# Kernel optimization log

Hardware: AMD Instinct MI355X
Metric: run time of the kernel (lower is better)

## Reference

```python
import jax, jax.numpy as jnp
import numpy as np

BS, N, D = 4, 512, 128

def setup_inputs() -> dict:
    key = jax.random.key(0)
    ks = jax.random.split(key, 8)
    s = 1.0 / np.sqrt(D)
    return {
        "x":  jax.random.normal(ks[0], (BS, N, D), dtype=jnp.float32),
        "Wq": jax.random.normal(ks[1], (D, D), dtype=jnp.float32) * s,
        "bq": jax.random.normal(ks[2], (D,), dtype=jnp.float32) * s,
        "Wk": jax.random.normal(ks[3], (D, D), dtype=jnp.float32) * s,
        "bk": jax.random.normal(ks[4], (D,), dtype=jnp.float32) * s,
        "Wv": jax.random.normal(ks[5], (D, D), dtype=jnp.float32) * s,
        "bv": jax.random.normal(ks[6], (D,), dtype=jnp.float32) * s,
        "pos_bias": jax.random.normal(ks[7], (N, N), dtype=jnp.float32) * 0.1,
    }

def reference(x, Wq, bq, Wk, bk, Wv, bv, pos_bias):
    # Linear projections (torch Linear: x @ W^T + b)
    q = jax.nn.sigmoid(jnp.einsum('bnd,ed->bne', x, Wq) + bq)   # [B,N,D]
    k = jnp.einsum('bnd,ed->bne', x, Wk) + bk                   # [B,N,D]
    v = jnp.einsum('bnd,ed->bne', x, Wv) + bv                   # [B,N,D]
    # scores[b,t,j,d] = k[b,j,d] + pos_bias[t,j]  (O(n^2 d) intermediate)
    s = k[:, None, :, :] + pos_bias[None, :, :, None]           # [B,N,N,D]
    m = jnp.max(s, axis=2, keepdims=True)                       # stabilizer
    e = jnp.exp(s - m)                                          # [B,N,N,D]
    num = jnp.einsum('btjd,bjd->btd', e, v)                     # [B,N,D]
    den = jnp.sum(e, axis=2)                                    # [B,N,D]
    return q * (num / den)
```

## Files before the change

kernel.cpp:

```cpp
#include <hip/hip_runtime.h>

#define BATCH 4
#define SEQ   512
#define DIM   128

typedef _Float16 half8 __attribute__((ext_vector_type(8)));
typedef _Float16 half4 __attribute__((ext_vector_type(4)));
typedef float    f32x4 __attribute__((ext_vector_type(4)));

__device__ __forceinline__ half8 ld8h(const float* __restrict__ p) {
    const float4 a = *(const float4*)p;
    const float4 b = *(const float4*)(p + 4);
    half8 h;
    h[0] = (_Float16)a.x; h[1] = (_Float16)a.y; h[2] = (_Float16)a.z; h[3] = (_Float16)a.w;
    h[4] = (_Float16)b.x; h[5] = (_Float16)b.y; h[6] = (_Float16)b.z; h[7] = (_Float16)b.w;
    return h;
}

__global__ __launch_bounds__(256) void KA(
    const float* __restrict__ x,
    const float* __restrict__ Wq, const float* __restrict__ bq,
    const float* __restrict__ Wk, const float* __restrict__ bk,
    const float* __restrict__ Wv, const float* __restrict__ bv,
    const float* __restrict__ pos,
    float* __restrict__ qout, _Float16* __restrict__ ekk,
    _Float16* __restrict__ ep_h)
{
    const int tid = threadIdx.x;
    const int bi  = blockIdx.x;

    if (bi >= 256) {
        const int i = ((bi - 256) * 256 + tid) * 8;
        const float4 p0 = *(const float4*)(pos + i);
        const float4 p1 = *(const float4*)(pos + i + 4);
        half8 h;
        h[0] = (_Float16)__expf(p0.x); h[1] = (_Float16)__expf(p0.y);
        h[2] = (_Float16)__expf(p0.z); h[3] = (_Float16)__expf(p0.w);
        h[4] = (_Float16)__expf(p1.x); h[5] = (_Float16)__expf(p1.y);
        h[6] = (_Float16)__expf(p1.z); h[7] = (_Float16)__expf(p1.w);
        *(half8*)(ep_h + i) = h;
        return;
    }

    const int lane = tid & 63;
    const int wave = tid >> 6;
    const int l15  = lane & 15;
    const int quad = lane >> 4;

    const int n0 = (bi & 7) * 16;
    const int m0 = (bi >> 3) * 64 + wave * 16;

    const float* xa = x  + (m0 + l15) * DIM + quad * 8;
    const float* wq = Wq + (n0 + l15) * DIM + quad * 8;
    const float* wk = Wk + (n0 + l15) * DIM + quad * 8;
    const float* wv = Wv + (n0 + l15) * DIM + quad * 8;

    f32x4 aq = {0.f, 0.f, 0.f, 0.f};
    f32x4 ak = {0.f, 0.f, 0.f, 0.f};
    f32x4 av = {0.f, 0.f, 0.f, 0.f};

#pragma unroll
    for (int ks = 0; ks < 4; ++ks) {
        const half8 a  = ld8h(xa + ks * 32);
        const half8 b0 = ld8h(wq + ks * 32);
        const half8 b1 = ld8h(wk + ks * 32);
        const half8 b2 = ld8h(wv + ks * 32);
        aq = __builtin_amdgcn_mfma_f32_16x16x32_f16(a, b0, aq, 0, 0, 0);
        ak = __builtin_amdgcn_mfma_f32_16x16x32_f16(a, b1, ak, 0, 0, 0);
        av = __builtin_amdgcn_mfma_f32_16x16x32_f16(a, b2, av, 0, 0, 0);
    }

    const int c = n0 + l15;
    const float bqv = bq[c];
    const float bkv = bk[c];
    const float bvv = bv[c];

    const int mrow = m0 + quad * 4;
    const int b    = mrow >> 9;
    const int tok  = mrow & 511;

    half4 eh, evh;
#pragma unroll
    for (int r = 0; r < 4; ++r) {
        const float e  = __expf(ak[r] + bkv);
        const float vv = av[r] + bvv;
        const float qv = 1.f / (1.f + __expf(-(aq[r] + bqv)));
        eh[r]  = (_Float16)e;
        evh[r] = (_Float16)(e * vv);
        qout[(b * SEQ + tok + r) * DIM + c] = qv;
    }
    *(half4*)(ekk + ((b * 256) + 2 * c + 0) * SEQ + tok) = eh;
    *(half4*)(ekk + ((b * 256) + 2 * c + 1) * SEQ + tok) = evh;
}

__global__ __launch_bounds__(256) void KB(
    const _Float16* __restrict__ ekk,
    const _Float16* __restrict__ ep_h,
    const float* __restrict__ qout,
    float* __restrict__ out)
{
    const int tid  = threadIdx.x;
    const int lane = tid & 63;
    const int wave = tid >> 6;
    const int l15  = lane & 15;
    const int quad = lane >> 4;

    const int bi = blockIdx.x;
    const int b  = bi >> 7;
    const int mt = (bi >> 4) & 7;
    const int tt = bi & 15;

    const int m0 = mt * 32 + (wave & 1) * 16;
    const int t0 = tt * 32 + (wave >> 1) * 16;

    const _Float16* arow = ekk  + ((b * 256) + m0 + l15) * SEQ + quad * 8;
    const _Float16* brow = ep_h + (t0 + l15) * SEQ + quad * 8;

    f32x4 acc = {0.f, 0.f, 0.f, 0.f};

#pragma unroll
    for (int ks = 0; ks < 16; ++ks) {
        const half8 a  = *(const half8*)(arow + ks * 32);
        const half8 b8 = *(const half8*)(brow + ks * 32);
        acc = __builtin_amdgcn_mfma_f32_16x16x32_f16(a, b8, acc, 0, 0, 0);
    }

    const int d0 = (m0 + quad * 4) >> 1;
    const int t  = t0 + l15;
    const float2 qv = *(const float2*)(qout + ((b * SEQ) + t) * DIM + d0);
    float2 o;
    o.x = qv.x * acc[1] / acc[0];
    o.y = qv.y * acc[3] / acc[2];
    *(float2*)(out + ((b * SEQ) + t) * DIM + d0) = o;
}

extern "C" void kernel_launch(void* const* d_in, const int* in_sizes, int n_in,
                              void* d_out, int out_size, void* d_ws, size_t ws_size,
                              hipStream_t stream) {
    const float* x   = (const float*)d_in[0];
    const float* Wq  = (const float*)d_in[1];
    const float* bq  = (const float*)d_in[2];
    const float* Wk  = (const float*)d_in[3];
    const float* bk  = (const float*)d_in[4];
    const float* Wv  = (const float*)d_in[5];
    const float* bv  = (const float*)d_in[6];
    const float* pos = (const float*)d_in[7];

    float* outp = (float*)d_out;
    char*  ws   = (char*)d_ws;

    _Float16* ekk  = (_Float16*)(ws);
    _Float16* ep_h = (_Float16*)(ws + (1024 << 10));
    float*    qout = (float*)   (ws + (1536 << 10));

    KA<<<384, 256, 0, stream>>>(x, Wq, bq, Wk, bk, Wv, bv, pos, qout, ekk, ep_h);
    KB<<<512, 256, 0, stream>>>(ekk, ep_h, qout, outp);
}
```

Before: 81.16 us.

## Fuse projection, exp and attention-sum into one kernel using LDS staging

Merges the two kernels into one. Each block recomputes exp(K) and exp(K)*V for its batch and 16-dim slice over all tokens, plus exp(pos_bias) for its 32 query rows, and stages them in padded shared memory before the MFMA reduction. This removes the global workspace round trip and a second launch. The cost is redundant recomputation of the K/V projection across the 16 query tiles, heavy L2 traffic for x, and large LDS use that limits occupancy.

```diff
diff --git a/kernel.cpp b/kernel.cpp
--- a/kernel.cpp
+++ b/kernel.cpp
@@ -3,6 +3,7 @@
 #define BATCH 4
 #define SEQ   512
 #define DIM   128
+#define PADJ  516
 
 typedef _Float16 half8 __attribute__((ext_vector_type(8)));
 typedef _Float16 half4 __attribute__((ext_vector_type(4)));
@@ -17,121 +18,137 @@
     return h;
 }
 
-__global__ __launch_bounds__(256) void KA(
+__global__ __launch_bounds__(256, 2) void k_fused(
     const float* __restrict__ x,
     const float* __restrict__ Wq, const float* __restrict__ bq,
     const float* __restrict__ Wk, const float* __restrict__ bk,
     const float* __restrict__ Wv, const float* __restrict__ bv,
     const float* __restrict__ pos,
-    float* __restrict__ qout, _Float16* __restrict__ ekk,
-    _Float16* __restrict__ ep_h)
-{
-    const int tid = threadIdx.x;
-    const int bi  = blockIdx.x;
-
-    if (bi >= 256) {
-        const int i = ((bi - 256) * 256 + tid) * 8;
-        const float4 p0 = *(const float4*)(pos + i);
-        const float4 p1 = *(const float4*)(pos + i + 4);
-        half8 h;
-        h[0] = (_Float16)__expf(p0.x); h[1] = (_Float16)__expf(p0.y);
-        h[2] = (_Float16)__expf(p0.z); h[3] = (_Float16)__expf(p0.w);
-        h[4] = (_Float16)__expf(p1.x); h[5] = (_Float16)__expf(p1.y);
-        h[6] = (_Float16)__expf(p1.z); h[7] = (_Float16)__expf(p1.w);
-        *(half8*)(ep_h + i) = h;
-        return;
-    }
-
-    const int lane = tid & 63;
-    const int wave = tid >> 6;
-    const int l15  = lane & 15;
-    const int quad = lane >> 4;
-
-    const int n0 = (bi & 7) * 16;
-    const int m0 = (bi >> 3) * 64 + wave * 16;
-
-    const float* xa = x  + (m0 + l15) * DIM + quad * 8;
-    const float* wq = Wq + (n0 + l15) * DIM + quad * 8;
-    const float* wk = Wk + (n0 + l15) * DIM + quad * 8;
-    const float* wv = Wv + (n0 + l15) * DIM + quad * 8;
-
-    f32x4 aq = {0.f, 0.f, 0.f, 0.f};
-    f32x4 ak = {0.f, 0.f, 0.f, 0.f};
-    f32x4 av = {0.f, 0.f, 0.f, 0.f};
-
-#pragma unroll
-    for (int ks = 0; ks < 4; ++ks) {
-        const half8 a  = ld8h(xa + ks * 32);
-        const half8 b0 = ld8h(wq + ks * 32);
-        const half8 b1 = ld8h(wk + ks * 32);
-        const half8 b2 = ld8h(wv + ks * 32);
-        aq = __builtin_amdgcn_mfma_f32_16x16x32_f16(a, b0, aq, 0, 0, 0);
-        ak = __builtin_amdgcn_mfma_f32_16x16x32_f16(a, b1, ak, 0, 0, 0);
-        av = __builtin_amdgcn_mfma_f32_16x16x32_f16(a, b2, av, 0, 0, 0);
-    }
-
-    const int c = n0 + l15;
-    const float bqv = bq[c];
-    const float bkv = bk[c];
-    const float bvv = bv[c];
-
-    const int mrow = m0 + quad * 4;
-    const int b    = mrow >> 9;
-    const int tok  = mrow & 511;
-
-    half4 eh, evh;
-#pragma unroll
-    for (int r = 0; r < 4; ++r) {
-        const float e  = __expf(ak[r] + bkv);
-        const float vv = av[r] + bvv;
-        const float qv = 1.f / (1.f + __expf(-(aq[r] + bqv)));
-        eh[r]  = (_Float16)e;
-        evh[r] = (_Float16)(e * vv);
-        qout[(b * SEQ + tok + r) * DIM + c] = qv;
-    }
-    *(half4*)(ekk + ((b * 256) + 2 * c + 0) * SEQ + tok) = eh;
-    *(half4*)(ekk + ((b * 256) + 2 * c + 1) * SEQ + tok) = evh;
-}
-
-__global__ __launch_bounds__(256) void KB(
-    const _Float16* __restrict__ ekk,
-    const _Float16* __restrict__ ep_h,
-    const float* __restrict__ qout,
     float* __restrict__ out)
 {
+    __shared__ _Float16 ekk_s[32 * PADJ];
+    __shared__ _Float16 ep_s [32 * PADJ];
+    __shared__ float    q_s  [32 * 16];
+
     const int tid  = threadIdx.x;
     const int lane = tid & 63;
     const int wave = tid >> 6;
     const int l15  = lane & 15;
     const int quad = lane >> 4;
 
-    const int bi = blockIdx.x;
-    const int b  = bi >> 7;
-    const int mt = (bi >> 4) & 7;
-    const int tt = bi & 15;
+    const int bi  = blockIdx.x;
+    const int b   = bi >> 7;
+    const int dt  = (bi >> 4) & 7;
+    const int tt  = bi & 15;
+    const int d0g = dt * 16;
+    const int t0g = tt * 32;
 
-    const int m0 = mt * 32 + (wave & 1) * 16;
-    const int t0 = tt * 32 + (wave >> 1) * 16;
+    const float* xb = x + b * SEQ * DIM;
 
-    const _Float16* arow = ekk  + ((b * 256) + m0 + l15) * SEQ + quad * 8;
-    const _Float16* brow = ep_h + (t0 + l15) * SEQ + quad * 8;
+    {
+        const int t  = tid >> 3;
+        const int j0 = (tid & 7) * 64;
+        const float* pr = pos + (t0g + t) * SEQ + j0;
+        _Float16* dst = ep_s + t * PADJ + j0;
+#pragma unroll
+        for (int u = 0; u < 64; u += 8) {
+            const float4 a = *(const float4*)(pr + u);
+            const float4 c = *(const float4*)(pr + u + 4);
+            half8 h;
+            h[0] = (_Float16)__expf(a.x); h[1] = (_Float16)__expf(a.y);
+            h[2] = (_Float16)__expf(a.z); h[3] = (_Float16)__expf(a.w);
+            h[4] = (_Float16)__expf(c.x); h[5] = (_Float16)__expf(c.y);
+            h[6] = (_Float16)__expf(c.z); h[7] = (_Float16)__expf(c.w);
+            *(half8*)(dst + u) = h;
+        }
+    }
 
-    f32x4 acc = {0.f, 0.f, 0.f, 0.f};
+    {
+        half8 wkf[4], wvf[4];
+        const float* wkr = Wk + (d0g + l15) * DIM + quad * 8;
+        const float* wvr = Wv + (d0g + l15) * DIM + quad * 8;
+#pragma unroll
+        for (int ks = 0; ks < 4; ++ks) {
+            wkf[ks] = ld8h(wkr + ks * 32);
+            wvf[ks] = ld8h(wvr + ks * 32);
+        }
+        const float bkv = bk[d0g + l15];
+        const float bvv = bv[d0g + l15];
+        const int tokbase = wave * 128;
 
 #pragma unroll
-    for (int ks = 0; ks < 16; ++ks) {
-        const half8 a  = *(const half8*)(arow + ks * 32);
-        const half8 b8 = *(const half8*)(brow + ks * 32);
-        acc = __builtin_amdgcn_mfma_f32_16x16x32_f16(a, b8, acc, 0, 0, 0);
+        for (int mt = 0; mt < 8; ++mt) {
+            f32x4 ak = {0.f, 0.f, 0.f, 0.f};
+            f32x4 av = {0.f, 0.f, 0.f, 0.f};
+            const float* xr = xb + (tokbase + mt * 16 + l15) * DIM + quad * 8;
+#pragma unroll
+            for (int ks = 0; ks < 4; ++ks) {
+                const half8 a = ld8h(xr + ks * 32);
+                ak = __builtin_amdgcn_mfma_f32_16x16x32_f16(a, wkf[ks], ak, 0, 0, 0);
+                av = __builtin_amdgcn_mfma_f32_16x16x32_f16(a, wvf[ks], av, 0, 0, 0);
+            }
+            const int j0r = tokbase + mt * 16 + quad * 4;
+            half4 eh, evh;
+#pragma unroll
+            for (int r = 0; r < 4; ++r) {
+                const float e = __expf(ak[r] + bkv);
+                eh[r]  = (_Float16)e;
+                evh[r] = (_Float16)(e * (av[r] + bvv));
+            }
+            *(half4*)(ekk_s + (2 * l15 + 0) * PADJ + j0r) = eh;
+            *(half4*)(ekk_s + (2 * l15 + 1) * PADJ + j0r) = evh;
+        }
     }
 
-    const int d0 = (m0 + quad * 4) >> 1;
-    const int t  = t0 + l15;
-    const float2 qv = *(const float2*)(qout + ((b * SEQ) + t) * DIM + d0);
+    if (wave < 2) {
+        half8 wqf[4];
+        const float* wqr = Wq + (d0g + l15) * DIM + quad * 8;
+#pragma unroll
+        for (int ks = 0; ks < 4; ++ks) wqf[ks] = ld8h(wqr + ks * 32);
+        const float bqv = bq[d0g + l15];
+        f32x4 aq = {0.f, 0.f, 0.f, 0.f};
+        const float* xr = xb + (t0g + wave * 16 + l15) * DIM + quad * 8;
+#pragma unroll
+        for (int ks = 0; ks < 4; ++ks) {
+            const half8 a = ld8h(xr + ks * 32);
+            aq = __builtin_amdgcn_mfma_f32_16x16x32_f16(a, wqf[ks], aq, 0, 0, 0);
+        }
+#pragma unroll
+        for (int r = 0; r < 4; ++r)
+            q_s[(wave * 16 + quad * 4 + r) * 16 + l15] =
+                1.f / (1.f + __expf(-(aq[r] + bqv)));
+    }
+
+    __syncthreads();
+
+    const int wm  = wave & 1;
+    const int wt  = wave >> 1;
+    const int m0w = wm * 16;
+    const int t0w = wt * 16;
+
+    const _Float16* arow = ekk_s + (m0w + l15) * PADJ + quad * 8;
+    const _Float16* brow = ep_s  + (t0w + l15) * PADJ + quad * 8;
+
+    f32x4 acc0 = {0.f, 0.f, 0.f, 0.f};
+    f32x4 acc1 = {0.f, 0.f, 0.f, 0.f};
+#pragma unroll
+    for (int ks = 0; ks < 16; ks += 2) {
+        const half8 a0 = *(const half8*)(arow + ks * 32);
+        const half8 b0 = *(const half8*)(brow + ks * 32);
+        const half8 a1 = *(const half8*)(arow + ks * 32 + 32);
+        const half8 b1 = *(const half8*)(brow + ks * 32 + 32);
+        acc0 = __builtin_amdgcn_mfma_f32_16x16x32_f16(a0, b0, acc0, 0, 0, 0);
+        acc1 = __builtin_amdgcn_mfma_f32_16x16x32_f16(a1, b1, acc1, 0, 0, 0);
+    }
+    const f32x4 acc = acc0 + acc1;
+
+    const int dl = (m0w + quad * 4) >> 1;
+    const int t  = t0w + l15;
+    const float2 qv = { q_s[t * 16 + dl], q_s[t * 16 + dl + 1] };
     float2 o;
     o.x = qv.x * acc[1] / acc[0];
     o.y = qv.y * acc[3] / acc[2];
-    *(float2*)(out + ((b * SEQ) + t) * DIM + d0) = o;
+    *(float2*)(out + (b * SEQ + t0g + t) * DIM + d0g + dl) = o;
 }
 
 extern "C" void kernel_launch(void* const* d_in, const int* in_sizes, int n_in,
@@ -146,13 +163,5 @@
     const float* bv  = (const float*)d_in[6];
     const float* pos = (const float*)d_in[7];
 
-    float* outp = (float*)d_out;
-    char*  ws   = (char*)d_ws;
-
-    _Float16* ekk  = (_Float16*)(ws);
-    _Float16* ep_h = (_Float16*)(ws + (1024 << 10));
-    float*    qout = (float*)   (ws + (1536 << 10));
-
-    KA<<<384, 256, 0, stream>>>(x, Wq, bq, Wk, bk, Wv, bv, pos, qout, ekk, ep_h);
-    KB<<<512, 256, 0, stream>>>(ekk, ep_h, qout, outp);
+    k_fused<<<512, 256, 0, stream>>>(x, Wq, bq, Wk, bk, Wv, bv, pos, (float*)d_out);
 }
```

Measured after the change: 96.74 us. 19.2% more time.
